# Kernel tuning notes

Measured on AMD Instinct MI355X. Metric: run time of the kernel, lower is better.

Reference implementation:

```python
import jax, jax.numpy as jnp
import numpy as np

SHAPES = ((64, 64), (32, 32), (16, 16))   # H/8, H/16, H/32 levels of a 512x512 image
B, D = 32, 256
NH, L, P = 8, 3, 4                        # MSDeformAttn heads / levels / points
DH = D // NH
NCLS, NC, NH_CA = 200, 10, 2
LQ = 32 * 32
LIN = sum(h * w for h, w in SHAPES)


def _ref_points():
    # get_reference_points for the H/16 grid, normalized (x, y) in (0,1)
    H_, W_ = 32, 32
    ry, rx = np.meshgrid(np.linspace(0.5, H_ - 0.5, H_) / H_,
                         np.linspace(0.5, W_ - 0.5, W_) / W_, indexing='ij')
    ref = np.stack([rx.ravel(), ry.ravel()], -1).astype(np.float32)  # (Lq, 2)
    return jnp.asarray(ref)[None, :, None, :]                        # (1, Lq, 1, 2)


def _msda(query, feats, W_off, b_off, W_attn, b_attn, W_val, b_val, W_out, b_out):
    """Multi-scale deformable attention (grid_sample bilinear, align_corners=False, zero pad)."""
    value = (feats @ W_val + b_val).reshape(B, LIN, NH, DH)
    off = (query @ W_off + b_off).reshape(B, LQ, NH, L, P, 2)
    aw = jax.nn.softmax((query @ W_attn + b_attn).reshape(B, LQ, NH, L * P), -1)
    aw = aw.reshape(B, LQ, NH, L, P)
    norm = jnp.asarray([[w, h] for h, w in SHAPES], jnp.float32)     # (L, 2) as (W, H)
    ref = _ref_points()                                              # (1, Lq, 1, 2)
    loc = ref[:, :, None, :, None, :] + off / norm[None, None, None, :, None, :]  # (B,Lq,NH,L,P,2)

    out = jnp.zeros((B, NH, LQ, DH), query.dtype)
    start = 0
    for lvl, (H_, W_) in enumerate(SHAPES):
        v = value[:, start:start + H_ * W_].transpose(0, 2, 1, 3)    # (B, NH, HW, DH)
        start += H_ * W_
        lx = loc[:, :, :, lvl, :, 0] * W_ - 0.5                      # (B, Lq, NH, P)
        ly = loc[:, :, :, lvl, :, 1] * H_ - 0.5
        x0 = jnp.floor(lx).astype(jnp.int32)
        y0 = jnp.floor(ly).astype(jnp.int32)
        dx = (lx - x0).transpose(0, 2, 1, 3)                         # (B, NH, Lq, P)
        dy = (ly - y0).transpose(0, 2, 1, 3)

        def gather(ix, iy):
            valid = (ix >= 0) & (ix < W_) & (iy >= 0) & (iy < H_)
            idx = (jnp.clip(iy, 0, H_ - 1) * W_ + jnp.clip(ix, 0, W_ - 1))
            idx = idx.transpose(0, 2, 1, 3).reshape(B, NH, LQ * P)
            g = jnp.take_along_axis(v, idx[..., None], axis=2).reshape(B, NH, LQ, P, DH)
            return g * valid.transpose(0, 2, 1, 3)[..., None]

        samp = (gather(x0,     y0)     * ((1 - dx) * (1 - dy))[..., None]
              + gather(x0 + 1, y0)     * (dx * (1 - dy))[..., None]
              + gather(x0,     y0 + 1) * ((1 - dx) * dy)[..., None]
              + gather(x0 + 1, y0 + 1) * (dx * dy)[..., None])       # (B,NH,Lq,P,DH)
        out = out + (samp * aw[:, :, :, lvl, :].transpose(0, 2, 1, 3)[..., None]).sum(3)
    out = out.transpose(0, 2, 1, 3).reshape(B, LQ, D)
    return out @ W_out + b_out


def _cross_attn(x, concepts, Wq, bq, Wkv, bkv, Wp, bp):
    Bx, N, _ = x.shape
    M = concepts.shape[1]
    dh = D // NH_CA
    q = (x @ Wq + bq).reshape(Bx, N, NH_CA, dh).transpose(0, 2, 1, 3)          # (B, h, N, dh)
    kv = (concepts @ Wkv + bkv).reshape(1, M, 2, NH_CA, dh).transpose(2, 0, 3, 1, 4)
    k, v = kv[0], kv[1]                                                        # (1, h, M, dh)
    attn = jax.nn.softmax(jnp.einsum('bhnd,ohmd->bhnm', q, k) * (dh ** -0.5), -1)
    o = jnp.einsum('bhnm,ohmd->bhnd', attn, v).transpose(0, 2, 1, 3).reshape(Bx, N, D)
    return o @ Wp + bp, attn


def _forward(query, feats, x_cls, W_off, b_off, W_attn, b_attn, W_val, b_val, W_out, b_out,
             unsup_concepts, concepts, spatial_concepts,
             Wq_c, bq_c, Wkv_c, bkv_c, Wp_c, bp_c,
             Wq_s, bq_s, Wkv_s, bkv_s, Wp_s, bp_s):
    # injector-style residual: query tokens refined by multi-scale deformable attention
    x = query + _msda(query, feats, W_off, b_off, W_attn, b_attn, W_val, b_val, W_out, b_out)
    # NB: original code reuses concept_tranformer for the unsup branch (faithful to source)
    out_u, attn_u = _cross_attn(x_cls, unsup_concepts, Wq_c, bq_c, Wkv_c, bkv_c, Wp_c, bp_c)
    out_n, attn_n = _cross_attn(x_cls, concepts,       Wq_c, bq_c, Wkv_c, bkv_c, Wp_c, bp_c)
    out_s, attn_s = _cross_attn(x,     spatial_concepts, Wq_s, bq_s, Wkv_s, bkv_s, Wp_s, bp_s)
    out = out_u[:, 0] + out_n[:, 0] + out_s.mean(1)                  # (B, num_classes)
    return out, attn_u.mean(1), attn_n.mean(1), attn_s.mean(1)


def setup_inputs() -> dict:
    key = jax.random.key(0)
    ks = jax.random.split(key, 20)
    s = 1.0 / np.sqrt(D)

    def n(i, shape, scale=1.0):
        return jax.random.normal(ks[i], shape, jnp.float32) * scale

    return dict(
        query=n(0, (B, LQ, D)), feats=n(1, (B, LIN, D)), x_cls=n(2, (B, 1, D)),
        W_off=n(3, (D, NH * L * P * 2), 0.01), b_off=n(4, (NH * L * P * 2,), 0.5),
        W_attn=n(5, (D, NH * L * P), 0.01), b_attn=jnp.zeros((NH * L * P,)),
        W_val=n(6, (D, D), s), b_val=jnp.zeros((D,)),
        W_out=n(7, (D, D), s), b_out=jnp.zeros((D,)),
        unsup_concepts=n(8, (1, NC, D), s), concepts=n(9, (1, NC, D), s),
        spatial_concepts=n(10, (1, NC, D), s),
        Wq_c=n(11, (D, D), s), bq_c=jnp.zeros((D,)),
        Wkv_c=n(12, (D, 2 * D), s), bkv_c=jnp.zeros((2 * D,)),
        Wp_c=n(13, (D, NCLS), s), bp_c=jnp.zeros((NCLS,)),
        Wq_s=n(14, (D, D), s), bq_s=jnp.zeros((D,)),
        Wkv_s=n(15, (D, 2 * D), s), bkv_s=jnp.zeros((2 * D,)),
        Wp_s=n(16, (D, NCLS), s), bp_s=jnp.zeros((NCLS,)),
    )


def reference(query, feats, x_cls, W_off, b_off, W_attn, b_attn, W_val, b_val, W_out, b_out,
              unsup_concepts, concepts, spatial_concepts,
              Wq_c, bq_c, Wkv_c, bkv_c, Wp_c, bp_c,
              Wq_s, bq_s, Wkv_s, bkv_s, Wp_s, bp_s):
    return _forward(query, feats, x_cls, W_off, b_off, W_attn, b_attn, W_val, b_val, W_out, b_out,
                    unsup_concepts, concepts, spatial_concepts,
                    Wq_c, bq_c, Wkv_c, bkv_c, Wp_c, bp_c,
                    Wq_s, bq_s, Wkv_s, bkv_s, Wp_s, bp_s)
```

## Files before the change

kernel.cpp:

```cpp
#include <hip/hip_runtime.h>
#include <hip/hip_bf16.h>


typedef __attribute__((ext_vector_type(8))) short s16x8;
typedef __attribute__((ext_vector_type(4))) float f32x4;

__device__ __forceinline__ void store_val(float* p, float v) { *p = v; }
__device__ __forceinline__ void store_val(__hip_bfloat16* p, float v) { *p = __float2bfloat16(v); }

__device__ __forceinline__ unsigned short f2bf(float x) {
  unsigned int u = __builtin_bit_cast(unsigned int, x);
  u += 0x7FFFu + ((u >> 16) & 1u);
  return (unsigned short)(u >> 16);
}
__device__ __forceinline__ float bf2f(unsigned short u) {
  return __builtin_bit_cast(float, (unsigned int)u << 16);
}
__device__ __forceinline__ float bflo(unsigned int u) {
  return __builtin_bit_cast(float, u << 16);
}
__device__ __forceinline__ float bfhi(unsigned int u) {
  return __builtin_bit_cast(float, u & 0xFFFF0000u);
}

__device__ __forceinline__ void gload16(const char* g, char* l) {
  __builtin_amdgcn_global_load_lds(
      (const __attribute__((address_space(1))) unsigned int*)g,
      (__attribute__((address_space(3))) unsigned int*)l, 16, 0, 0);
}

__global__ __launch_bounds__(256) void prep_all(
    const float* __restrict__ W_val, const float* __restrict__ W_off,
    const float* __restrict__ b_off, const float* __restrict__ W_attn,
    const float* __restrict__ b_attn, char* __restrict__ imgV,
    char* __restrict__ imgQ, float* __restrict__ bpack,
    const float* __restrict__ unsup, const float* __restrict__ conc,
    const float* __restrict__ spat, const float* __restrict__ Wkv_c,
    const float* __restrict__ bkv_c, const float* __restrict__ Wkv_s,
    const float* __restrict__ bkv_s, float* __restrict__ kv_u,
    float* __restrict__ kv_n, float* __restrict__ kv_s,
    const float* __restrict__ Wq_s, const float* __restrict__ bq_s,
    const float* __restrict__ W_out, const float* __restrict__ b_out,
    float* __restrict__ WLt, float* __restrict__ WL2t, float* __restrict__ cL)
{
  const int bi = blockIdx.x;
  const int tid = threadIdx.x;
  if (bi <= 576) {
    const int n = bi, k = tid;
    if (n == 576) {
      bpack[k] = (k < 192) ? b_off[k] : ((k < 288) ? b_attn[k - 192] : 0.f);
      if (k < 64) bpack[256 + k] = (k < 32) ? b_attn[64 + k] : 0.f;
      return;
    }
    const int ks = k >> 6;
    const int kb = (k & 63) * 2;
    if (n < 256) {
      const unsigned short v = f2bf(W_val[(size_t)k * 256 + n]);
      *(unsigned short*)(imgV + ks * 32768 + n * 128 + (kb ^ ((n & 7) << 4))) = v;
    } else {
      const int c = n - 256;
      float v = 0.f;
      if (c < 192) v = W_off[(size_t)k * 192 + c];
      else if (c < 288) v = W_attn[(size_t)k * 96 + (c - 192)];
      *(unsigned short*)(imgQ + ks * 40960 + c * 128 + (kb ^ ((c & 7) << 4))) = f2bf(v);
    }
    return;
  }
  if (bi <= 579) {
    const int j = bi - 577;
    const float* src = (j == 0) ? unsup : ((j == 1) ? conc : spat);
    const float* W   = (j < 2) ? Wkv_c : Wkv_s;
    const float* bb  = (j < 2) ? bkv_c : bkv_s;
    float* dst       = (j == 0) ? kv_u : ((j == 1) ? kv_n : kv_s);
    __shared__ float s[2560];
    for (int i = tid; i < 2560; i += 256) s[i] = src[i];
    __syncthreads();
    for (int o = tid; o < 5120; o += 256) {
      const int m = o >> 9, n = o & 511;
      float acc = bb[n];
      for (int k = 0; k < 256; ++k) acc += s[m * 256 + k] * W[(size_t)k * 512 + n];
      dst[o] = acc;
    }
    return;
  }
  {
    const int j = bi - 580;
    const int h = j / 10, m = j % 10;
    __shared__ float kk[128], wl[256], bred[256];
    if (tid < 128) {
      const int n = h * 128 + tid;
      float acc = bkv_s[n];
      for (int k = 0; k < 256; ++k) acc += spat[m * 256 + k] * Wkv_s[(size_t)k * 512 + n];
      kk[tid] = acc;
    }
    __syncthreads();
    float acc = 0.f;
    for (int e = 0; e < 128; ++e) acc += Wq_s[(size_t)tid * 256 + h * 128 + e] * kk[e];
    wl[tid] = acc;
    __syncthreads();
    float acc2 = 0.f;
    for (int t = 0; t < 256; ++t) acc2 += W_out[(size_t)tid * 256 + t] * wl[t];
    const float scale = 0.08838834764831845f;
    WLt[j * 256 + tid] = scale * acc;
    WL2t[j * 256 + tid] = scale * acc2;
    bred[tid] = b_out[tid] * wl[tid] + ((tid < 128) ? bq_s[h * 128 + tid] * kk[tid] : 0.f);
    __syncthreads();
    for (int s = 128; s > 0; s >>= 1) {
      if (tid < s) bred[tid] += bred[tid + s];
      __syncthreads();
    }
    if (tid == 0) cL[j] = scale * bred[0];
  }
}

template <typename OT, int NCOLS, int MINW>
__global__ __launch_bounds__(512, MINW) void gemm_f32a(
    const float* __restrict__ A, const char* __restrict__ Bimg,
    const float* __restrict__ bias, OT* __restrict__ C)
{
  constexpr int NFR = NCOLS / 64;
  __shared__ char sAf[32768];
  __shared__ char sBb[NCOLS * 128];

  const int tid = threadIdx.x;
  const int lane = tid & 63;
  const int w = tid >> 6;
  const int wr = (w >> 2) * 64;
  const int wc = (w & 3) * (NCOLS / 4);
  const int l15 = lane & 15;
  const int lg = lane >> 4;
  const int m0 = blockIdx.x * 128;

  int asrc[4];
#pragma unroll
  for (int i = 0; i < 4; ++i) {
    const int slot = w * 256 + i * 64 + lane;
    const int row = slot >> 4;
    const int c = (slot & 15) ^ (row & 7);
    asrc[i] = row * 256 + c * 4;
  }
  const float* Abase = A + (size_t)m0 * 256;

  f32x4 acc[4][NFR] = {};

#pragma unroll
  for (int ks = 0; ks < 4; ++ks) {
    if (ks) __syncthreads();
    {
      char* la = sAf + w * 4096;
#pragma unroll
      for (int i = 0; i < 4; ++i)
        gload16((const char*)(Abase + ks * 64 + asrc[i]), la + i * 1024);
      const char* gb = Bimg + ks * (NCOLS * 128) + w * (NCOLS * 16) + lane * 16;
      char* lb = sBb + w * (NCOLS * 16);
#pragma unroll
      for (int i = 0; i < NFR; ++i)
        gload16(gb + i * 1024, lb + i * 1024);
    }
    __syncthreads();
#pragma unroll
    for (int kk = 0; kk < 2; ++kk) {
      const int c0 = kk * 8 + lg * 2;
      s16x8 af[4];
#pragma unroll
      for (int mf = 0; mf < 4; ++mf) {
        const int row = wr + mf * 16 + l15;
        const int sw = row & 7;
        const f32x4 lo = *reinterpret_cast<const f32x4*>(
            sAf + row * 256 + ((c0 ^ sw) * 16));
        const f32x4 hi = *reinterpret_cast<const f32x4*>(
            sAf + row * 256 + (((c0 + 1) ^ sw) * 16));
        uint4 u;
        u.x = (unsigned)f2bf(lo[0]) | ((unsigned)f2bf(lo[1]) << 16);
        u.y = (unsigned)f2bf(lo[2]) | ((unsigned)f2bf(lo[3]) << 16);
        u.z = (unsigned)f2bf(hi[0]) | ((unsigned)f2bf(hi[1]) << 16);
        u.w = (unsigned)f2bf(hi[2]) | ((unsigned)f2bf(hi[3]) << 16);
        af[mf] = __builtin_bit_cast(s16x8, u);
      }
      const int kb = kk * 64 + lg * 16;
      s16x8 bf[NFR];
#pragma unroll
      for (int nf = 0; nf < NFR; ++nf) {
        const int col = wc + nf * 16 + l15;
        bf[nf] = *reinterpret_cast<const s16x8*>(sBb + col * 128 + (kb ^ ((col & 7) << 4)));
      }
#pragma unroll
      for (int mf = 0; mf < 4; ++mf)
#pragma unroll
        for (int nf = 0; nf < NFR; ++nf)
          acc[mf][nf] = __builtin_amdgcn_mfma_f32_16x16x32_bf16(af[mf], bf[nf], acc[mf][nf], 0, 0, 0);
    }
  }

#pragma unroll
  for (int nf = 0; nf < NFR; ++nf) {
    const int col = wc + nf * 16 + l15;
    const float bb = bias[col];
#pragma unroll
    for (int mf = 0; mf < 4; ++mf) {
#pragma unroll
      for (int j = 0; j < 4; ++j) {
        const int row = m0 + wr + mf * 16 + lg * 4 + j;
        store_val(&C[(size_t)row * NCOLS + col], acc[mf][nf][j] + bb);
      }
    }
  }
}

__global__ __launch_bounds__(256) void msda_v4(
    const float* __restrict__ offlog, const __hip_bfloat16* __restrict__ value,
    __hip_bfloat16* __restrict__ msda_out)
{
  const int bq0 = blockIdx.x * 8;
  const int b = bq0 >> 10;
  const int tid = threadIdx.x;
  __shared__ float aw[768];
  __shared__ int4 sRow[768];
  __shared__ float4 sW[768];
  __shared__ __align__(16) char gbuf[4 * 3 * 4096];

  if (tid < 64) {
    const int qi = tid >> 3, h = tid & 7;
    const float* lp = &offlog[(size_t)(bq0 + qi) * 320 + 192 + h * 12];
    float e[12];
    float mx = -1e30f;
#pragma unroll
    for (int i = 0; i < 12; ++i) { e[i] = lp[i]; mx = fmaxf(mx, e[i]); }
    float s = 0.f;
#pragma unroll
    for (int i = 0; i < 12; ++i) { e[i] = expf(e[i] - mx); s += e[i]; }
    const float inv = 1.f / s;
#pragma unroll
    for (int i = 0; i < 12; ++i) aw[qi * 96 + h * 12 + i] = e[i] * inv;
  }
  __syncthreads();

#pragma unroll
  for (int k = 0; k < 3; ++k) {
    const int j = k * 256 + tid;
    const int qi = j / 96, cc = j - qi * 96;
    const int q = (bq0 + qi) & 1023;
    const int h = cc / 12, r = cc - h * 12, l = r >> 2, p_ = r & 3;
    const int WHl[3] = {64, 32, 16};
    const int St[3] = {0, 4096, 5120};
    const float2 o2 = *reinterpret_cast<const float2*>(
        &offlog[(size_t)(bq0 + qi) * 320 + h * 24 + l * 8 + p_ * 2]);
    const float refx = ((q & 31) + 0.5f) * (1.0f / 32.0f);
    const float refy = ((q >> 5) + 0.5f) * (1.0f / 32.0f);
    const int WH = WHl[l];
    const float fw = (float)WH;
    const float lx = (refx + o2.x / fw) * fw - 0.5f;
    const float ly = (refy + o2.y / fw) * fw - 0.5f;
    const float fx = floorf(lx), fy = floorf(ly);
    const int x0 = (int)fx, y0 = (int)fy;
    const float dx = lx - fx, dy = ly - fy;
    const float a = aw[j];
    int rows[4];
    float ws[4];
#pragma unroll
    for (int c = 0; c < 4; ++c) {
      const int ix = x0 + (c & 1), iy = y0 + (c >> 1);
      const float wb = ((c & 1) ? dx : 1.f - dx) * ((c >> 1) ? dy : 1.f - dy);
      const bool valid = (ix >= 0) && (ix < WH) && (iy >= 0) && (iy < WH);
      const int cx = min(max(ix, 0), WH - 1);
      const int cy = min(max(iy, 0), WH - 1);
      rows[c] = St[l] + cy * WH + cx;
      ws[c] = valid ? wb * a : 0.f;
    }
    sRow[j] = int4{rows[0], rows[1], rows[2], rows[3]};
    sW[j] = float4{ws[0], ws[1], ws[2], ws[3]};
  }
  __syncthreads();

  const int w = tid >> 6;
  const int lane = tid & 63;
  const int qi = tid >> 5;
  const int h = (tid >> 2) & 7;
  const int d4 = tid & 3;
  const unsigned short* vb = (const unsigned short*)value
      + (size_t)b * (5376 * 256) + h * 32 + d4 * 8;
  const int cbase = qi * 96 + h * 12;
  char* gb = gbuf + w * 12288;

#pragma unroll
  for (int s0 = 0; s0 < 2; ++s0) {
    const int4 rows = sRow[cbase + s0];
    const int ra[4] = {rows.x, rows.y, rows.z, rows.w};
#pragma unroll
    for (int c = 0; c < 4; ++c)
      gload16((const char*)(vb + (size_t)ra[c] * 256), gb + s0 * 4096 + c * 1024);
  }

  float acc[8] = {};
#pragma unroll
  for (int s = 0; s < 12; ++s) {
    if (s + 2 < 12) {
      const int4 rows = sRow[cbase + s + 2];
      const int ra[4] = {rows.x, rows.y, rows.z, rows.w};
      const int slot = (s + 2) % 3;
#pragma unroll
      for (int c = 0; c < 4; ++c)
        gload16((const char*)(vb + (size_t)ra[c] * 256), gb + slot * 4096 + c * 1024);
    }
    if (s <= 9)       asm volatile("s_waitcnt vmcnt(8)" ::: "memory");
    else if (s == 10) asm volatile("s_waitcnt vmcnt(4)" ::: "memory");
    else              asm volatile("s_waitcnt vmcnt(0)" ::: "memory");
    __builtin_amdgcn_sched_barrier(0);
    const float4 wv = sW[cbase + s];
    const float wa[4] = {wv.x, wv.y, wv.z, wv.w};
    const int slot = s % 3;
#pragma unroll
    for (int c = 0; c < 4; ++c) {
      const uint4 v = *reinterpret_cast<const uint4*>(gb + slot * 4096 + c * 1024 + lane * 16);
      const float wgt = wa[c];
      acc[0] += wgt * bflo(v.x); acc[1] += wgt * bfhi(v.x);
      acc[2] += wgt * bflo(v.y); acc[3] += wgt * bfhi(v.y);
      acc[4] += wgt * bflo(v.z); acc[5] += wgt * bfhi(v.z);
      acc[6] += wgt * bflo(v.w); acc[7] += wgt * bfhi(v.w);
    }
  }
  uint4 o;
  o.x = (unsigned)f2bf(acc[0]) | ((unsigned)f2bf(acc[1]) << 16);
  o.y = (unsigned)f2bf(acc[2]) | ((unsigned)f2bf(acc[3]) << 16);
  o.z = (unsigned)f2bf(acc[4]) | ((unsigned)f2bf(acc[5]) << 16);
  o.w = (unsigned)f2bf(acc[6]) | ((unsigned)f2bf(acc[7]) << 16);
  *reinterpret_cast<uint4*>(
      (unsigned short*)msda_out + (size_t)(bq0 + qi) * 256 + h * 32 + d4 * 8) = o;
}

__global__ __launch_bounds__(256) void spatial_kernel(
    const float* __restrict__ query, const __hip_bfloat16* __restrict__ msda,
    const float* __restrict__ WLt, const float* __restrict__ WL2t,
    const float* __restrict__ cL, float* __restrict__ attn_out,
    float* __restrict__ partial)
{
  __shared__ float wls[20][256];
  __shared__ float wl2s[20][256];
  __shared__ float red[128][20];
  const int tid = threadIdx.x;
  for (int i = tid; i < 5120; i += 256) {
    wls[i >> 8][i & 255] = WLt[i];
    wl2s[i >> 8][i & 255] = WL2t[i];
  }
  const int row_local = tid >> 1;
  const int half = tid & 1;
  const int row = blockIdx.x * 128 + row_local;
  float acc[20];
#pragma unroll
  for (int c = 0; c < 20; ++c) acc[c] = half ? 0.f : cL[c];
  __syncthreads();

  const float* qp = &query[(size_t)row * 256 + half * 128];
  const unsigned short* mp = (const unsigned short*)msda + (size_t)row * 256 + half * 128;
  const int kbase = half * 128;
  for (int k = 0; k < 128; k += 4) {
    const f32x4 q4 = *reinterpret_cast<const f32x4*>(qp + k);
    const uint2 mm = *reinterpret_cast<const uint2*>(mp + k);
    const float m0 = bf2f((unsigned short)mm.x);
    const float m1 = bf2f((unsigned short)(mm.x >> 16));
    const float m2 = bf2f((unsigned short)mm.y);
    const float m3 = bf2f((unsigned short)(mm.y >> 16));
#pragma unroll
    for (int c = 0; c < 20; ++c) {
      const f32x4 w4 = *reinterpret_cast<const f32x4*>(&wls[c][kbase + k]);
      const f32x4 v4 = *reinterpret_cast<const f32x4*>(&wl2s[c][kbase + k]);
      acc[c] += q4.x * w4.x + q4.y * w4.y + q4.z * w4.z + q4.w * w4.w
              + m0 * v4.x + m1 * v4.y + m2 * v4.z + m3 * v4.w;
    }
  }
  if (half == 1) {
#pragma unroll
    for (int c = 0; c < 20; ++c) red[row_local][c] = acc[c];
  }
  __syncthreads();
  if (half == 0) {
    float a[20];
#pragma unroll
    for (int c = 0; c < 20; ++c) a[c] = acc[c] + red[row_local][c];
#pragma unroll
    for (int h = 0; h < 2; ++h) {
      float mx = -1e30f;
#pragma unroll
      for (int m = 0; m < 10; ++m) mx = fmaxf(mx, a[h * 10 + m]);
      float s = 0.f;
#pragma unroll
      for (int m = 0; m < 10; ++m) { a[h * 10 + m] = expf(a[h * 10 + m] - mx); s += a[h * 10 + m]; }
      const float inv = 1.f / s;
#pragma unroll
      for (int m = 0; m < 10; ++m) a[h * 10 + m] *= inv;
    }
#pragma unroll
    for (int m = 0; m < 10; ++m)
      attn_out[(size_t)row * 10 + m] = 0.5f * (a[m] + a[10 + m]);
#pragma unroll
    for (int c = 0; c < 20; ++c) red[row_local][c] = a[c];
  }
  __syncthreads();
  if (tid < 20) {
    float s = 0.f;
    for (int r = 0; r < 128; ++r) s += red[r][tid];
    partial[blockIdx.x * 20 + tid] = s;
  }
}

__global__ __launch_bounds__(256) void final2_kernel(
    const float* __restrict__ x_cls, const float* __restrict__ Wq_c,
    const float* __restrict__ bq_c, const float* __restrict__ kv_u,
    const float* __restrict__ kv_n, const float* __restrict__ partial,
    const float* __restrict__ kv_s, const float* __restrict__ Wp_c,
    const float* __restrict__ bp_c, const float* __restrict__ Wp_s,
    const float* __restrict__ bp_s, float* __restrict__ out,
    float* __restrict__ attn_u_out, float* __restrict__ attn_n_out)
{
  const int b = blockIdx.x, tid = threadIdx.x;
  __shared__ float ou[256], osb[256], abar[20], xr[256];
  if (tid < 64)
    *reinterpret_cast<float4*>(&xr[tid * 4]) =
        *reinterpret_cast<const float4*>(&x_cls[(size_t)b * 256 + tid * 4]);
  if (tid >= 64 && tid < 84) {
    const int c = tid - 64;
    float s = 0.f;
    for (int ch = 0; ch < 8; ++ch) s += partial[(b * 8 + ch) * 20 + c];
    abar[c] = s * (1.0f / 1024.0f);
  }
  __syncthreads();
  if (tid < 64) {
    const int lane = tid;
    float4 q4 = *reinterpret_cast<const float4*>(&bq_c[lane * 4]);
    for (int k = 0; k < 256; ++k) {
      const float xk = xr[k];
      const float4 w = *reinterpret_cast<const float4*>(&Wq_c[(size_t)k * 256 + lane * 4]);
      q4.x += xk * w.x; q4.y += xk * w.y; q4.z += xk * w.z; q4.w += xk * w.w;
    }
    const float scale = 0.08838834764831845f;
    float4 osum = {0.f, 0.f, 0.f, 0.f};
    for (int cs = 0; cs < 2; ++cs) {
      const float* kv = cs ? kv_n : kv_u;
      float* aout = cs ? attn_n_out : attn_u_out;
      float attn[10];
      float mx = -1e30f;
#pragma unroll
      for (int m = 0; m < 10; ++m) {
        const float4 k4 = *reinterpret_cast<const float4*>(&kv[m * 512 + lane * 4]);
        float p = q4.x * k4.x + q4.y * k4.y + q4.z * k4.z + q4.w * k4.w;
        p += __shfl_xor(p, 1);  p += __shfl_xor(p, 2);  p += __shfl_xor(p, 4);
        p += __shfl_xor(p, 8);  p += __shfl_xor(p, 16);
        attn[m] = p * scale;
        mx = fmaxf(mx, attn[m]);
      }
      float s = 0.f;
#pragma unroll
      for (int m = 0; m < 10; ++m) { attn[m] = expf(attn[m] - mx); s += attn[m]; }
      const float inv = 1.f / s;
#pragma unroll
      for (int m = 0; m < 10; ++m) {
        attn[m] *= inv;
        const float am = 0.5f * (attn[m] + __shfl_xor(attn[m], 32));
        if (lane == m) aout[b * 10 + m] = am;
        const float4 v4 = *reinterpret_cast<const float4*>(&kv[m * 512 + 256 + lane * 4]);
        osum.x += attn[m] * v4.x; osum.y += attn[m] * v4.y;
        osum.z += attn[m] * v4.z; osum.w += attn[m] * v4.w;
      }
    }
    *reinterpret_cast<float4*>(&ou[lane * 4]) = osum;
  }
  {
    const int h = tid >> 7, d = tid & 127;
    float s = 0.f;
#pragma unroll
    for (int m = 0; m < 10; ++m) s += abar[h * 10 + m] * kv_s[m * 512 + 256 + h * 128 + d];
    osb[tid] = s;
  }
  __syncthreads();
  if (tid < 200) {
    float acc = 2.f * bp_c[tid] + bp_s[tid];
    for (int dd = 0; dd < 256; ++dd)
      acc += ou[dd] * Wp_c[dd * 200 + tid] + osb[dd] * Wp_s[dd * 200 + tid];
    out[b * 200 + tid] = acc;
  }
}

extern "C" void kernel_launch(void* const* d_in, const int* in_sizes, int n_in,
                              void* d_out, int out_size, void* d_ws, size_t ws_size,
                              hipStream_t stream)
{
  const float* query  = (const float*)d_in[0];
  const float* feats  = (const float*)d_in[1];
  const float* x_cls  = (const float*)d_in[2];
  const float* W_off  = (const float*)d_in[3];
  const float* b_off  = (const float*)d_in[4];
  const float* W_attn = (const float*)d_in[5];
  const float* b_attn = (const float*)d_in[6];
  const float* W_val  = (const float*)d_in[7];
  const float* b_val  = (const float*)d_in[8];
  const float* W_out  = (const float*)d_in[9];
  const float* b_out  = (const float*)d_in[10];
  const float* unsup  = (const float*)d_in[11];
  const float* conc   = (const float*)d_in[12];
  const float* spat   = (const float*)d_in[13];
  const float* Wq_c   = (const float*)d_in[14];
  const float* bq_c   = (const float*)d_in[15];
  const float* Wkv_c  = (const float*)d_in[16];
  const float* bkv_c  = (const float*)d_in[17];
  const float* Wp_c   = (const float*)d_in[18];
  const float* bp_c   = (const float*)d_in[19];
  const float* Wq_s   = (const float*)d_in[20];
  const float* bq_s   = (const float*)d_in[21];
  const float* Wkv_s  = (const float*)d_in[22];
  const float* bkv_s  = (const float*)d_in[23];
  const float* Wp_s   = (const float*)d_in[24];
  const float* bp_s   = (const float*)d_in[25];
  float* out = (float*)d_out;

  const int B = 32, LQ = 1024, LIN = 5376;
  const int MQ = B * LQ;
  const int MV = B * LIN;

  char* p = (char*)d_ws;
  __hip_bfloat16* value = (__hip_bfloat16*)p;   p += (size_t)MV * 256 * 2;
  float* offlog   = (float*)p;                  p += (size_t)MQ * 320 * 4;
  __hip_bfloat16* msda = (__hip_bfloat16*)p;    p += (size_t)MQ * 256 * 2;
  char* imgV      = p;                          p += 4 * 32768;
  char* imgQ      = p;                          p += 4 * 40960;
  float* bpack    = (float*)p;                  p += 320 * 4;
  float* kv_u     = (float*)p;                  p += 5120 * 4;
  float* kv_n     = (float*)p;                  p += 5120 * 4;
  float* kv_s     = (float*)p;                  p += 5120 * 4;
  float* WLt      = (float*)p;                  p += 5120 * 4;
  float* WL2t     = (float*)p;                  p += 5120 * 4;
  float* cL       = (float*)p;                  p += 32 * 4;
  float* partial  = (float*)p;                  p += 256 * 20 * 4;

  dim3 blk(256);
  prep_all<<<dim3(600), blk, 0, stream>>>(
      W_val, W_off, b_off, W_attn, b_attn, imgV, imgQ, bpack,
      unsup, conc, spat, Wkv_c, bkv_c, Wkv_s, bkv_s, kv_u, kv_n, kv_s,
      Wq_s, bq_s, W_out, b_out, WLt, WL2t, cL);
  gemm_f32a<__hip_bfloat16, 256, 4><<<dim3(MV / 128), dim3(512), 0, stream>>>(
      feats, imgV, b_val, value);
  gemm_f32a<float, 320, 2><<<dim3(MQ / 128), dim3(512), 0, stream>>>(
      query, imgQ, bpack, offlog);
  msda_v4<<<dim3(MQ / 8), blk, 0, stream>>>(offlog, value, msda);
  spatial_kernel<<<dim3(MQ / 128), blk, 0, stream>>>(
      query, msda, WLt, WL2t, cL, out + 7040, partial);
  final2_kernel<<<dim3(B), blk, 0, stream>>>(
      x_cls, Wq_c, bq_c, kv_u, kv_n, partial, kv_s, Wp_c, bp_c, Wp_s, bp_s,
      out, out + 6400, out + 6720);
}
```

Measured before the change: 320.3 us.

## Merge value and offset GEMMs into one launch, shrink MSDA staging

Measured after the change: 331.6 us. 3.5% more time.

```diff
diff --git a/kernel.cpp b/kernel.cpp
--- a/kernel.cpp
+++ b/kernel.cpp
@@ -113,23 +113,19 @@
   }
 }
 
-template <typename OT, int NCOLS, int MINW>
-__global__ __launch_bounds__(512, MINW) void gemm_f32a(
+template <typename OT, int NCOLS, int NOUT>
+__device__ __forceinline__ void gemm_body(
     const float* __restrict__ A, const char* __restrict__ Bimg,
-    const float* __restrict__ bias, OT* __restrict__ C)
+    const float* __restrict__ bias, OT* __restrict__ C, int m0,
+    char* sAf, char* sBb, int tid)
 {
   constexpr int NFR = NCOLS / 64;
-  __shared__ char sAf[32768];
-  __shared__ char sBb[NCOLS * 128];
-
-  const int tid = threadIdx.x;
   const int lane = tid & 63;
   const int w = tid >> 6;
   const int wr = (w >> 2) * 64;
   const int wc = (w & 3) * (NCOLS / 4);
   const int l15 = lane & 15;
   const int lg = lane >> 4;
-  const int m0 = blockIdx.x * 128;
 
   int asrc[4];
 #pragma unroll
@@ -195,19 +191,36 @@
 #pragma unroll
   for (int nf = 0; nf < NFR; ++nf) {
     const int col = wc + nf * 16 + l15;
+    if (col >= NOUT) continue;
     const float bb = bias[col];
 #pragma unroll
     for (int mf = 0; mf < 4; ++mf) {
 #pragma unroll
       for (int j = 0; j < 4; ++j) {
         const int row = m0 + wr + mf * 16 + lg * 4 + j;
-        store_val(&C[(size_t)row * NCOLS + col], acc[mf][nf][j] + bb);
+        store_val(&C[(size_t)row * NOUT + col], acc[mf][nf][j] + bb);
       }
     }
   }
 }
 
-__global__ __launch_bounds__(256) void msda_v4(
+__global__ __launch_bounds__(512, 2) void gemm_merged(
+    const float* __restrict__ feats, const char* __restrict__ imgV,
+    const float* __restrict__ b_val, __hip_bfloat16* __restrict__ value,
+    const float* __restrict__ query, const char* __restrict__ imgQ,
+    const float* __restrict__ bpack, float* __restrict__ offlog)
+{
+  __shared__ char sAf[32768];
+  __shared__ char sBb[320 * 128];
+  if (blockIdx.x < 1344)
+    gemm_body<__hip_bfloat16, 256, 256>(feats, imgV, b_val, value,
+                                        blockIdx.x * 128, sAf, sBb, threadIdx.x);
+  else
+    gemm_body<float, 320, 288>(query, imgQ, bpack, offlog,
+                               (blockIdx.x - 1344) * 128, sAf, sBb, threadIdx.x);
+}
+
+__global__ __launch_bounds__(256) void msda_v5(
     const float* __restrict__ offlog, const __hip_bfloat16* __restrict__ value,
     __hip_bfloat16* __restrict__ msda_out)
 {
@@ -215,13 +228,13 @@
   const int b = bq0 >> 10;
   const int tid = threadIdx.x;
   __shared__ float aw[768];
-  __shared__ int4 sRow[768];
+  __shared__ ushort4 sRowU[768];
   __shared__ float4 sW[768];
-  __shared__ __align__(16) char gbuf[4 * 3 * 4096];
+  __shared__ __align__(16) char gbuf[4 * 2 * 4096];
 
   if (tid < 64) {
     const int qi = tid >> 3, h = tid & 7;
-    const float* lp = &offlog[(size_t)(bq0 + qi) * 320 + 192 + h * 12];
+    const float* lp = &offlog[(size_t)(bq0 + qi) * 288 + 192 + h * 12];
     float e[12];
     float mx = -1e30f;
 #pragma unroll
@@ -244,7 +257,7 @@
     const int WHl[3] = {64, 32, 16};
     const int St[3] = {0, 4096, 5120};
     const float2 o2 = *reinterpret_cast<const float2*>(
-        &offlog[(size_t)(bq0 + qi) * 320 + h * 24 + l * 8 + p_ * 2]);
+        &offlog[(size_t)(bq0 + qi) * 288 + h * 24 + l * 8 + p_ * 2]);
     const float refx = ((q & 31) + 0.5f) * (1.0f / 32.0f);
     const float refy = ((q >> 5) + 0.5f) * (1.0f / 32.0f);
     const int WH = WHl[l];
@@ -255,7 +268,7 @@
     const int x0 = (int)fx, y0 = (int)fy;
     const float dx = lx - fx, dy = ly - fy;
     const float a = aw[j];
-    int rows[4];
+    unsigned short rows[4];
     float ws[4];
 #pragma unroll
     for (int c = 0; c < 4; ++c) {
@@ -264,10 +277,10 @@
       const bool valid = (ix >= 0) && (ix < WH) && (iy >= 0) && (iy < WH);
       const int cx = min(max(ix, 0), WH - 1);
       const int cy = min(max(iy, 0), WH - 1);
-      rows[c] = St[l] + cy * WH + cx;
+      rows[c] = (unsigned short)(St[l] + cy * WH + cx);
       ws[c] = valid ? wb * a : 0.f;
     }
-    sRow[j] = int4{rows[0], rows[1], rows[2], rows[3]};
+    sRowU[j] = ushort4{rows[0], rows[1], rows[2], rows[3]};
     sW[j] = float4{ws[0], ws[1], ws[2], ws[3]};
   }
   __syncthreads();
@@ -280,35 +293,34 @@
   const unsigned short* vb = (const unsigned short*)value
       + (size_t)b * (5376 * 256) + h * 32 + d4 * 8;
   const int cbase = qi * 96 + h * 12;
-  char* gb = gbuf + w * 12288;
-
-#pragma unroll
-  for (int s0 = 0; s0 < 2; ++s0) {
-    const int4 rows = sRow[cbase + s0];
+  char* gb = gbuf + w * 8192;
+
+  {
+    const ushort4 rows = sRowU[cbase];
     const int ra[4] = {rows.x, rows.y, rows.z, rows.w};
 #pragma unroll
     for (int c = 0; c < 4; ++c)
-      gload16((const char*)(vb + (size_t)ra[c] * 256), gb + s0 * 4096 + c * 1024);
+      gload16((const char*)(vb + (size_t)ra[c] * 256), gb + c * 1024);
   }
 
   float acc[8] = {};
 #pragma unroll
   for (int s = 0; s < 12; ++s) {
-    if (s + 2 < 12) {
-      const int4 rows = sRow[cbase + s + 2];
+    if (s + 1 < 12) {
+      const ushort4 rows = sRowU[cbase + s + 1];
       const int ra[4] = {rows.x, rows.y, rows.z, rows.w};
-      const int slot = (s + 2) % 3;
+      const int slot = (s + 1) & 1;
 #pragma unroll
       for (int c = 0; c < 4; ++c)
         gload16((const char*)(vb + (size_t)ra[c] * 256), gb + slot * 4096 + c * 1024);
-    }
-    if (s <= 9)       asm volatile("s_waitcnt vmcnt(8)" ::: "memory");
-    else if (s == 10) asm volatile("s_waitcnt vmcnt(4)" ::: "memory");
-    else              asm volatile("s_waitcnt vmcnt(0)" ::: "memory");
+      asm volatile("s_waitcnt vmcnt(4)" ::: "memory");
+    } else {
+      asm volatile("s_waitcnt vmcnt(0)" ::: "memory");
+    }
     __builtin_amdgcn_sched_barrier(0);
     const float4 wv = sW[cbase + s];
     const float wa[4] = {wv.x, wv.y, wv.z, wv.w};
-    const int slot = s % 3;
+    const int slot = s & 1;
 #pragma unroll
     for (int c = 0; c < 4; ++c) {
       const uint4 v = *reinterpret_cast<const uint4*>(gb + slot * 4096 + c * 1024 + lane * 16);
@@ -518,7 +530,7 @@
 
   char* p = (char*)d_ws;
   __hip_bfloat16* value = (__hip_bfloat16*)p;   p += (size_t)MV * 256 * 2;
-  float* offlog   = (float*)p;                  p += (size_t)MQ * 320 * 4;
+  float* offlog   = (float*)p;                  p += (size_t)MQ * 288 * 4;
   __hip_bfloat16* msda = (__hip_bfloat16*)p;    p += (size_t)MQ * 256 * 2;
   char* imgV      = p;                          p += 4 * 32768;
   char* imgQ      = p;                          p += 4 * 40960;
@@ -536,11 +548,9 @@
       W_val, W_off, b_off, W_attn, b_attn, imgV, imgQ, bpack,
       unsup, conc, spat, Wkv_c, bkv_c, Wkv_s, bkv_s, kv_u, kv_n, kv_s,
       Wq_s, bq_s, W_out, b_out, WLt, WL2t, cL);
-  gemm_f32a<__hip_bfloat16, 256, 4><<<dim3(MV / 128), dim3(512), 0, stream>>>(
-      feats, imgV, b_val, value);
-  gemm_f32a<float, 320, 2><<<dim3(MQ / 128), dim3(512), 0, stream>>>(
-      query, imgQ, bpack, offlog);
-  msda_v4<<<dim3(MQ / 8), blk, 0, stream>>>(offlog, value, msda);
+  gemm_merged<<<dim3(1600), dim3(512), 0, stream>>>(
+      feats, imgV, b_val, value, query, imgQ, bpack, offlog);
+  msda_v5<<<dim3(MQ / 8), blk, 0, stream>>>(offlog, value, msda);
   spatial_kernel<<<dim3(MQ / 128), blk, 0, stream>>>(
       query, msda, WLt, WL2t, cL, out + 7040, partial);
   final2_kernel<<<dim3(B), blk, 0, stream>>>(
```

## Merge value and query GEMMs into one double-buffered pipelined kernel

Applied to the files above, without the earlier changes.

Measured after the change: 329.9 us. +3.0%, slower.

```diff
diff --git a/kernel.cpp b/kernel.cpp
--- a/kernel.cpp
+++ b/kernel.cpp
@@ -52,17 +52,19 @@
       if (k < 64) bpack[256 + k] = (k < 32) ? b_attn[64 + k] : 0.f;
       return;
     }
-    const int ks = k >> 6;
-    const int kb = (k & 63) * 2;
+    const int ks = k >> 5;
+    const int kb = (k & 31) * 2;
     if (n < 256) {
-      const unsigned short v = f2bf(W_val[(size_t)k * 256 + n]);
-      *(unsigned short*)(imgV + ks * 32768 + n * 128 + (kb ^ ((n & 7) << 4))) = v;
+      const int sw = ((n >> 1) & 3) << 4;
+      *(unsigned short*)(imgV + ks * 16384 + n * 64 + (kb ^ sw)) =
+          f2bf(W_val[(size_t)k * 256 + n]);
     } else {
       const int c = n - 256;
       float v = 0.f;
       if (c < 192) v = W_off[(size_t)k * 192 + c];
       else if (c < 288) v = W_attn[(size_t)k * 96 + (c - 192)];
-      *(unsigned short*)(imgQ + ks * 40960 + c * 128 + (kb ^ ((c & 7) << 4))) = f2bf(v);
+      const int sw = ((c >> 1) & 3) << 4;
+      *(unsigned short*)(imgQ + ks * 20480 + c * 64 + (kb ^ sw)) = f2bf(v);
     }
     return;
   }
@@ -113,98 +115,128 @@
   }
 }
 
-template <typename OT, int NCOLS, int MINW>
-__global__ __launch_bounds__(512, MINW) void gemm_f32a(
+template <typename OT, int NCOLS, int NOUT>
+__device__ __forceinline__ void gemm_body2(
     const float* __restrict__ A, const char* __restrict__ Bimg,
-    const float* __restrict__ bias, OT* __restrict__ C)
+    const float* __restrict__ bias, OT* __restrict__ C, int m0,
+    char* sA , char* sB , int tid)
 {
   constexpr int NFR = NCOLS / 64;
-  __shared__ char sAf[32768];
-  __shared__ char sBb[NCOLS * 128];
-
-  const int tid = threadIdx.x;
+  constexpr int BSTEP = NCOLS * 64;
   const int lane = tid & 63;
   const int w = tid >> 6;
   const int wr = (w >> 2) * 64;
   const int wc = (w & 3) * (NCOLS / 4);
   const int l15 = lane & 15;
   const int lg = lane >> 4;
-  const int m0 = blockIdx.x * 128;
-
-  int asrc[4];
-#pragma unroll
-  for (int i = 0; i < 4; ++i) {
-    const int slot = w * 256 + i * 64 + lane;
-    const int row = slot >> 4;
-    const int c = (slot & 15) ^ (row & 7);
+
+  int asrc[2];
+#pragma unroll
+  for (int i = 0; i < 2; ++i) {
+    const int slot = w * 128 + i * 64 + lane;
+    const int row = slot >> 3;
+    const int c = (slot & 7) ^ (row & 7);
     asrc[i] = row * 256 + c * 4;
   }
   const float* Abase = A + (size_t)m0 * 256;
 
   f32x4 acc[4][NFR] = {};
 
-#pragma unroll
-  for (int ks = 0; ks < 4; ++ks) {
-    if (ks) __syncthreads();
-    {
-      char* la = sAf + w * 4096;
-#pragma unroll
-      for (int i = 0; i < 4; ++i)
-        gload16((const char*)(Abase + ks * 64 + asrc[i]), la + i * 1024);
-      const char* gb = Bimg + ks * (NCOLS * 128) + w * (NCOLS * 16) + lane * 16;
-      char* lb = sBb + w * (NCOLS * 16);
-#pragma unroll
-      for (int i = 0; i < NFR; ++i)
-        gload16(gb + i * 1024, lb + i * 1024);
-    }
-    __syncthreads();
-#pragma unroll
-    for (int kk = 0; kk < 2; ++kk) {
-      const int c0 = kk * 8 + lg * 2;
-      s16x8 af[4];
-#pragma unroll
-      for (int mf = 0; mf < 4; ++mf) {
-        const int row = wr + mf * 16 + l15;
-        const int sw = row & 7;
-        const f32x4 lo = *reinterpret_cast<const f32x4*>(
-            sAf + row * 256 + ((c0 ^ sw) * 16));
-        const f32x4 hi = *reinterpret_cast<const f32x4*>(
-            sAf + row * 256 + (((c0 + 1) ^ sw) * 16));
-        uint4 u;
-        u.x = (unsigned)f2bf(lo[0]) | ((unsigned)f2bf(lo[1]) << 16);
-        u.y = (unsigned)f2bf(lo[2]) | ((unsigned)f2bf(lo[3]) << 16);
-        u.z = (unsigned)f2bf(hi[0]) | ((unsigned)f2bf(hi[1]) << 16);
-        u.w = (unsigned)f2bf(hi[2]) | ((unsigned)f2bf(hi[3]) << 16);
-        af[mf] = __builtin_bit_cast(s16x8, u);
+  auto issue = [&](int s) {
+    char* la = sA + (s & 1) * 16384 + w * 2048;
+    const float* Ab = Abase + s * 32;
+    gload16((const char*)(Ab + asrc[0]), la);
+    gload16((const char*)(Ab + asrc[1]), la + 1024);
+    const char* gb = Bimg + (size_t)s * BSTEP + lane * 16;
+    char* lb = sB + (s & 1) * BSTEP;
+#pragma unroll
+    for (int i = 0; i < 2; ++i)
+      gload16(gb + (w * 2 + i) * 1024, lb + (w * 2 + i) * 1024);
+    if constexpr (NFR == 5) {
+      if (w < 4)
+        gload16(gb + (16 + w) * 1024, lb + (16 + w) * 1024);
+    }
+  };
+
+  issue(0);
+#pragma unroll
+  for (int s = 0; s < 8; ++s) {
+    if (s) __builtin_amdgcn_s_barrier();
+    if (s < 7) {
+      issue(s + 1);
+      if constexpr (NFR == 5) {
+        if (w < 4) asm volatile("s_waitcnt vmcnt(5)" ::: "memory");
+        else       asm volatile("s_waitcnt vmcnt(4)" ::: "memory");
+      } else {
+        asm volatile("s_waitcnt vmcnt(4)" ::: "memory");
       }
-      const int kb = kk * 64 + lg * 16;
-      s16x8 bf[NFR];
-#pragma unroll
-      for (int nf = 0; nf < NFR; ++nf) {
-        const int col = wc + nf * 16 + l15;
-        bf[nf] = *reinterpret_cast<const s16x8*>(sBb + col * 128 + (kb ^ ((col & 7) << 4)));
-      }
-#pragma unroll
-      for (int mf = 0; mf < 4; ++mf)
-#pragma unroll
-        for (int nf = 0; nf < NFR; ++nf)
-          acc[mf][nf] = __builtin_amdgcn_mfma_f32_16x16x32_bf16(af[mf], bf[nf], acc[mf][nf], 0, 0, 0);
-    }
+    } else {
+      asm volatile("s_waitcnt vmcnt(0)" ::: "memory");
+    }
+    __builtin_amdgcn_s_barrier();
+    __builtin_amdgcn_sched_barrier(0);
+    const char* la = sA + (s & 1) * 16384;
+    const char* lb = sB + (s & 1) * BSTEP;
+    const int c0 = lg * 2;
+    s16x8 af[4];
+#pragma unroll
+    for (int mf = 0; mf < 4; ++mf) {
+      const int row = wr + mf * 16 + l15;
+      const int sw = row & 7;
+      const f32x4 lo = *reinterpret_cast<const f32x4*>(la + row * 128 + ((c0 ^ sw) * 16));
+      const f32x4 hi = *reinterpret_cast<const f32x4*>(la + row * 128 + (((c0 + 1) ^ sw) * 16));
+      uint4 u;
+      u.x = (unsigned)f2bf(lo[0]) | ((unsigned)f2bf(lo[1]) << 16);
+      u.y = (unsigned)f2bf(lo[2]) | ((unsigned)f2bf(lo[3]) << 16);
+      u.z = (unsigned)f2bf(hi[0]) | ((unsigned)f2bf(hi[1]) << 16);
+      u.w = (unsigned)f2bf(hi[2]) | ((unsigned)f2bf(hi[3]) << 16);
+      af[mf] = __builtin_bit_cast(s16x8, u);
+    }
+    const int kb = lg * 16;
+    s16x8 bf[NFR];
+#pragma unroll
+    for (int nf = 0; nf < NFR; ++nf) {
+      const int col = wc + nf * 16 + l15;
+      bf[nf] = *reinterpret_cast<const s16x8*>(
+          lb + col * 64 + (kb ^ (((col >> 1) & 3) << 4)));
+    }
+#pragma unroll
+    for (int mf = 0; mf < 4; ++mf)
+#pragma unroll
+      for (int nf = 0; nf < NFR; ++nf)
+        acc[mf][nf] = __builtin_amdgcn_mfma_f32_16x16x32_bf16(af[mf], bf[nf], acc[mf][nf], 0, 0, 0);
   }
 
 #pragma unroll
   for (int nf = 0; nf < NFR; ++nf) {
     const int col = wc + nf * 16 + l15;
+    if (col >= NOUT) continue;
     const float bb = bias[col];
 #pragma unroll
     for (int mf = 0; mf < 4; ++mf) {
 #pragma unroll
       for (int j = 0; j < 4; ++j) {
         const int row = m0 + wr + mf * 16 + lg * 4 + j;
-        store_val(&C[(size_t)row * NCOLS + col], acc[mf][nf][j] + bb);
+        store_val(&C[(size_t)row * NOUT + col], acc[mf][nf][j] + bb);
       }
     }
   }
+}
+
+__global__ __launch_bounds__(512, 2) void gemm_merged(
+    const float* __restrict__ feats, const char* __restrict__ imgV,
+    const float* __restrict__ b_val, __hip_bfloat16* __restrict__ value,
+    const float* __restrict__ query, const char* __restrict__ imgQ,
+    const float* __restrict__ bpack, float* __restrict__ offlog)
+{
+  __shared__ char sA[2 * 16384];
+  __shared__ char sB[2 * 320 * 64];
+  if (blockIdx.x < 1344)
+    gemm_body2<__hip_bfloat16, 256, 256>(feats, imgV, b_val, value,
+                                         blockIdx.x * 128, sA, sB, threadIdx.x);
+  else
+    gemm_body2<float, 320, 288>(query, imgQ, bpack, offlog,
+                                (blockIdx.x - 1344) * 128, sA, sB, threadIdx.x);
 }
 
 __global__ __launch_bounds__(256) void msda_v4(
@@ -221,7 +253,7 @@
 
   if (tid < 64) {
     const int qi = tid >> 3, h = tid & 7;
-    const float* lp = &offlog[(size_t)(bq0 + qi) * 320 + 192 + h * 12];
+    const float* lp = &offlog[(size_t)(bq0 + qi) * 288 + 192 + h * 12];
     float e[12];
     float mx = -1e30f;
 #pragma unroll
@@ -244,7 +276,7 @@
     const int WHl[3] = {64, 32, 16};
     const int St[3] = {0, 4096, 5120};
     const float2 o2 = *reinterpret_cast<const float2*>(
-        &offlog[(size_t)(bq0 + qi) * 320 + h * 24 + l * 8 + p_ * 2]);
+        &offlog[(size_t)(bq0 + qi) * 288 + h * 24 + l * 8 + p_ * 2]);
     const float refx = ((q & 31) + 0.5f) * (1.0f / 32.0f);
     const float refy = ((q >> 5) + 0.5f) * (1.0f / 32.0f);
     const int WH = WHl[l];
@@ -518,10 +550,10 @@
 
   char* p = (char*)d_ws;
   __hip_bfloat16* value = (__hip_bfloat16*)p;   p += (size_t)MV * 256 * 2;
-  float* offlog   = (float*)p;                  p += (size_t)MQ * 320 * 4;
+  float* offlog   = (float*)p;                  p += (size_t)MQ * 288 * 4;
   __hip_bfloat16* msda = (__hip_bfloat16*)p;    p += (size_t)MQ * 256 * 2;
-  char* imgV      = p;                          p += 4 * 32768;
-  char* imgQ      = p;                          p += 4 * 40960;
+  char* imgV      = p;                          p += 8 * 16384;
+  char* imgQ      = p;                          p += 8 * 20480;
   float* bpack    = (float*)p;                  p += 320 * 4;
   float* kv_u     = (float*)p;                  p += 5120 * 4;
   float* kv_n     = (float*)p;                  p += 5120 * 4;
@@ -536,10 +568,8 @@
       W_val, W_off, b_off, W_attn, b_attn, imgV, imgQ, bpack,
       unsup, conc, spat, Wkv_c, bkv_c, Wkv_s, bkv_s, kv_u, kv_n, kv_s,
       Wq_s, bq_s, W_out, b_out, WLt, WL2t, cL);
-  gemm_f32a<__hip_bfloat16, 256, 4><<<dim3(MV / 128), dim3(512), 0, stream>>>(
-      feats, imgV, b_val, value);
-  gemm_f32a<float, 320, 2><<<dim3(MQ / 128), dim3(512), 0, stream>>>(
-      query, imgQ, bpack, offlog);
+  gemm_merged<<<dim3(1600), dim3(512), 0, stream>>>(
+      feats, imgV, b_val, value, query, imgQ, bpack, offlog);
   msda_v4<<<dim3(MQ / 8), blk, 0, stream>>>(offlog, value, msda);
   spatial_kernel<<<dim3(MQ / 128), blk, 0, stream>>>(
       query, msda, WLt, WL2t, cL, out + 7040, partial);
```
